# Optimization experiments

Measured on AMD Instinct MI355X. Metric: run time of the kernel, lower is better.

The kernel has to match this reference:

```python
import jax, jax.numpy as jnp
import numpy as np

B, LQ, LKV = 4, 512, 8192
Q_DIM, KV_DIM = 1024, 512
QK_CH, V_CH, N_HEADS = 256, 256, 8
EPS = 1e-5


def _layernorm(x, g, b):
    m = jnp.mean(x, axis=-1, keepdims=True)
    v = jnp.mean(jnp.square(x - m), axis=-1, keepdims=True)
    return (x - m) * jax.lax.rsqrt(v + EPS) * g + b


def setup_inputs() -> dict:
    key = jax.random.key(0)
    ks = jax.random.split(key, 8)
    hidden_states = jax.random.normal(ks[0], (B, LQ, Q_DIM), dtype=jnp.float32)
    inputs = jax.random.normal(ks[1], (B, LKV, KV_DIM), dtype=jnp.float32)
    # Linear weights stored as [in, out] for x @ W
    Wq = jax.random.normal(ks[2], (Q_DIM, QK_CH), dtype=jnp.float32) * (1.0 / np.sqrt(Q_DIM))
    Wk = jax.random.normal(ks[3], (KV_DIM, QK_CH), dtype=jnp.float32) * (1.0 / np.sqrt(KV_DIM))
    Wv = jax.random.normal(ks[4], (KV_DIM, V_CH), dtype=jnp.float32) * (1.0 / np.sqrt(KV_DIM))
    bq = jnp.zeros((QK_CH,), jnp.float32)
    bk = jax.random.normal(ks[5], (QK_CH,), dtype=jnp.float32) * 0.02
    bv = jax.random.normal(ks[6], (V_CH,), dtype=jnp.float32) * 0.02
    ln1_g = jnp.ones((Q_DIM,), jnp.float32)
    ln1_b = jnp.zeros((Q_DIM,), jnp.float32)
    ln2_g = jnp.ones((KV_DIM,), jnp.float32)
    ln2_b = jnp.zeros((KV_DIM,), jnp.float32)
    return dict(hidden_states=hidden_states, inputs=inputs,
                ln1_g=ln1_g, ln1_b=ln1_b, ln2_g=ln2_g, ln2_b=ln2_b,
                Wq=Wq, bq=bq, Wk=Wk, bk=bk, Wv=Wv, bv=bv)


def reference(hidden_states, inputs, ln1_g, ln1_b, ln2_g, ln2_b,
              Wq, bq, Wk, bk, Wv, bv):
    H = N_HEADS
    dqk = QK_CH // H
    dv = V_CH // H
    hs = _layernorm(hidden_states, ln1_g, ln1_b)          # [B,LQ,Q_DIM]
    inp = _layernorm(inputs, ln2_g, ln2_b)                # [B,LKV,KV_DIM]
    q = (hs @ Wq + bq).reshape(B, LQ, H, dqk)             # [B,LQ,H,dqk]
    k = (inp @ Wk + bk).reshape(B, LKV, H, dqk)           # [B,LKV,H,dqk]
    v = (inp @ Wv + bv).reshape(B, LKV, H, dv)            # [B,LKV,H,dv]
    scores = jnp.einsum('bqhd,bkhd->bhqk', q, k) / np.sqrt(dqk).astype(np.float32)
    probs = jax.nn.softmax(scores, axis=-1)               # [B,H,LQ,LKV] (materialized, as in torch)
    ctx = jnp.einsum('bhqk,bkhd->bqhd', probs, v)         # [B,LQ,H,dv]
    return ctx.reshape(B, LQ, H * dv)
```

## Files before the change

### kernel.cpp

```cpp
#include <hip/hip_runtime.h>
#include <hip/hip_bf16.h>
#include <math.h>

#define NB    4
#define LQ    512
#define LKV   8192
#define QDIM  1024
#define KVDIM 512
#define NH    8
#define EPS_LN 1e-5f
#define SMAX  12.0f

typedef __attribute__((ext_vector_type(8))) short bf16x8;
typedef __attribute__((ext_vector_type(4))) float f32x4;

static __device__ __forceinline__ ushort f2bf(float x) {
    unsigned int u = __builtin_bit_cast(unsigned int, x);
    u += 0x7FFFu + ((u >> 16) & 1u);
    return (ushort)(u >> 16);
}

#if __has_builtin(__builtin_amdgcn_cvt_pk_bf16_f32)
static __device__ __forceinline__ unsigned int pk_bf16(float a, float b) {
    auto r = __builtin_amdgcn_cvt_pk_bf16_f32(a, b);
    return __builtin_bit_cast(unsigned int, r);
}
#else
static __device__ __forceinline__ unsigned int pk_bf16(float a, float b) {
    return (unsigned int)f2bf(a) | ((unsigned int)f2bf(b) << 16);
}
#endif

#if __has_builtin(__builtin_amdgcn_exp2f)
#define EXP2F(x) __builtin_amdgcn_exp2f(x)
#else
#define EXP2F(x) exp2f(x)
#endif

static __device__ __forceinline__ void interleave_swap(unsigned int &x, unsigned int &y, int lane) {
#if __has_builtin(__builtin_amdgcn_permlane32_swap) && __has_builtin(__builtin_amdgcn_permlane16_swap)
    {
        auto r1 = __builtin_amdgcn_permlane32_swap(x, y, false, false);
        auto r2 = __builtin_amdgcn_permlane16_swap(r1[0], r1[1], false, false);
        x = (unsigned int)r2[0];
        y = (unsigned int)r2[1];
    }
#else
    {
        unsigned int xs = (unsigned int)__shfl_xor((int)x, 32, 64);
        unsigned int ys = (unsigned int)__shfl_xor((int)y, 32, 64);
        unsigned int A2 = (lane & 32) ? ys : x;
        unsigned int C2 = (lane & 32) ? y  : xs;
        unsigned int A2x = (unsigned int)__shfl_xor((int)A2, 16, 64);
        unsigned int C2x = (unsigned int)__shfl_xor((int)C2, 16, 64);
        x = (lane & 16) ? C2x : A2;
        y = (lane & 16) ? C2  : A2x;
    }
#endif
}

static __device__ __forceinline__ void gld_lds16(const ushort* g, ushort* l) {
    __builtin_amdgcn_global_load_lds(
        (const __attribute__((address_space(1))) unsigned int*)g,
        (__attribute__((address_space(3))) unsigned int*)l, 16, 0, 0);
}

template<int K>
static __device__ __forceinline__ void ln_norm_row(
    const float* __restrict__ x, const float* __restrict__ g,
    const float* __restrict__ bta, ushort* __restrict__ y, int row, int lane)
{
    const float* xp = x + (size_t)row * K;
    constexpr int NV = K / 256;
    float4 v[NV];
    float s = 0.f;
#pragma unroll
    for (int i = 0; i < NV; ++i) {
        v[i] = *(const float4*)(xp + lane * 4 + i * 256);
        s += v[i].x + v[i].y + v[i].z + v[i].w;
    }
#pragma unroll
    for (int o = 1; o < 64; o <<= 1) s += __shfl_xor(s, o, 64);
    const float mu = s * (1.0f / K);
    float vs = 0.f;
#pragma unroll
    for (int i = 0; i < NV; ++i) {
        float dx = v[i].x - mu, dy = v[i].y - mu, dz = v[i].z - mu, dw = v[i].w - mu;
        vs += dx * dx + dy * dy + dz * dz + dw * dw;
    }
#pragma unroll
    for (int o = 1; o < 64; o <<= 1) vs += __shfl_xor(vs, o, 64);
    const float rs = rsqrtf(vs * (1.0f / K) + EPS_LN);
#pragma unroll
    for (int i = 0; i < NV; ++i) {
        const float4 gv = *(const float4*)(g   + lane * 4 + i * 256);
        const float4 bv = *(const float4*)(bta + lane * 4 + i * 256);
        uint2 o;
        o.x = pk_bf16((v[i].x - mu) * rs * gv.x + bv.x, (v[i].y - mu) * rs * gv.y + bv.y);
        o.y = pk_bf16((v[i].z - mu) * rs * gv.z + bv.z, (v[i].w - mu) * rs * gv.w + bv.w);
        *(uint2*)(y + (size_t)row * K + lane * 4 + i * 256) = o;
    }
}

static __device__ __forceinline__ void ln_stats_row(
    const float* __restrict__ x, float* __restrict__ mean, float* __restrict__ rstd,
    int row, int lane)
{
    const float* xp = x + (size_t)row * QDIM;
    float4 v[4];
    float s = 0.f;
#pragma unroll
    for (int i = 0; i < 4; ++i) {
        v[i] = *(const float4*)(xp + lane * 4 + i * 256);
        s += v[i].x + v[i].y + v[i].z + v[i].w;
    }
#pragma unroll
    for (int o = 1; o < 64; o <<= 1) s += __shfl_xor(s, o, 64);
    const float mu = s * (1.0f / QDIM);
    float vs = 0.f;
#pragma unroll
    for (int i = 0; i < 4; ++i) {
        float dx = v[i].x - mu, dy = v[i].y - mu, dz = v[i].z - mu, dw = v[i].w - mu;
        vs += dx * dx + dy * dy + dz * dz + dw * dw;
    }
#pragma unroll
    for (int o = 1; o < 64; o <<= 1) vs += __shfl_xor(vs, o, 64);
    if (lane == 0) {
        mean[row] = mu;
        rstd[row] = rsqrtf(vs * (1.0f / QDIM) + EPS_LN);
    }
}

static __device__ __forceinline__ void wt_transpose_body(
    const float* __restrict__ src, ushort* __restrict__ dst, int K,
    int kx, int ny, int t, ushort (*Ts)[72])
{
    const int k0 = kx * 64, n0 = ny * 64;
    const int nl = t & 63;
#pragma unroll
    for (int p = 0; p < 16; ++p) {
        const int kl = p * 4 + (t >> 6);
        Ts[nl][kl] = f2bf(src[(size_t)(k0 + kl) * 256 + n0 + nl]);
    }
    __syncthreads();
    const int ck = (t & 7) * 8;
#pragma unroll
    for (int p = 0; p < 2; ++p) {
        const int rn = p * 32 + (t >> 3);
        *(bf16x8*)(dst + (size_t)(n0 + rn) * K + k0 + ck) = *(const bf16x8*)&Ts[rn][ck];
    }
}

__global__ __launch_bounds__(256) void phaseA_kernel(
    const float* __restrict__ inputs, const float* __restrict__ ln2g,
    const float* __restrict__ ln2b,   ushort* __restrict__ Abf,
    const float* __restrict__ hidden, float* __restrict__ mean_h, float* __restrict__ rstd_h,
    const float* __restrict__ Wq, const float* __restrict__ Wk, const float* __restrict__ Wv,
    ushort* __restrict__ WtQ, ushort* __restrict__ WtKV)
{
    __shared__ ushort Ts[64][72];
    const int bid = blockIdx.x;
    const int t = threadIdx.x;
    const int lane = t & 63;
    if (bid < 8192) {
        ln_norm_row<KVDIM>(inputs, ln2g, ln2b, Abf, bid * 4 + (t >> 6), lane);
    } else if (bid < 8704) {
        ln_stats_row(hidden, mean_h, rstd_h, (bid - 8192) * 4 + (t >> 6), lane);
    } else if (bid < 8768) {
        const int p = bid - 8704;
        wt_transpose_body(Wq, WtQ, QDIM, p & 15, p >> 4, t, Ts);
    } else if (bid < 8800) {
        const int p = bid - 8768;
        wt_transpose_body(Wk, WtKV, KVDIM, p & 7, p >> 3, t, Ts);
    } else {
        const int p = bid - 8800;
        wt_transpose_body(Wv, WtKV + (size_t)256 * KVDIM, KVDIM, p & 7, p >> 3, t, Ts);
    }
}

__global__ __launch_bounds__(256) void phaseB_kernel(
    const ushort* __restrict__ Abf, const ushort* __restrict__ WtKV,
    const float* __restrict__ bk, const float* __restrict__ bv,
    ushort* __restrict__ kb, ushort* __restrict__ vt,
    const float* __restrict__ hidden, const float* __restrict__ mean_h,
    const float* __restrict__ rstd_h,
    const float* __restrict__ ln1g, const float* __restrict__ ln1b,
    const ushort* __restrict__ WtQ, const float* __restrict__ bq,
    ushort* __restrict__ qb, float oscale)
{
    __shared__ __align__(16) ushort SMEM[4 * 64 * 72];
    const int bid  = blockIdx.x;
    const int t    = threadIdx.x;
    const int lane = t & 63;
    const int w    = t >> 6;
    const int lq   = lane & 15;
    const int lg   = lane >> 4;
    const int wm   = w >> 1;
    const int wn   = w & 1;

    if (bid < 1024) {
        const int bm = (bid >> 2) * 128;
        const int bn = (bid & 3) * 128;
        ushort* As = SMEM;
        ushort* Bs = SMEM + 8192;

        const int srow = t >> 3;
        const int scol = ((t & 7) ^ (srow & 7)) * 8;
        const ushort* gA = Abf  + (size_t)(bm + srow) * KVDIM + scol;
        const ushort* gB = WtKV + (size_t)(bn + srow) * KVDIM + scol;

        f32x4 acc[4][4] = {};
        for (int k0 = 0; k0 < KVDIM; k0 += 64) {
#pragma unroll
            for (int p = 0; p < 4; ++p) {
                gld_lds16(gA + (size_t)(p * 32) * KVDIM + k0, As + p * 2048 + t * 8);
                gld_lds16(gB + (size_t)(p * 32) * KVDIM + k0, Bs + p * 2048 + t * 8);
            }
            __syncthreads();
#pragma unroll
            for (int kh = 0; kh < 2; ++kh) {
                bf16x8 af[4], bf[4];
#pragma unroll
                for (int mt = 0; mt < 4; ++mt) {
                    const int m = wm * 64 + mt * 16 + lq;
                    af[mt] = *(const bf16x8*)(As + m * 64 + (((lg + 4 * kh) ^ (m & 7)) << 3));
                }
#pragma unroll
                for (int nt = 0; nt < 4; ++nt) {
                    const int n = wn * 64 + nt * 16 + lq;
                    bf[nt] = *(const bf16x8*)(Bs + n * 64 + (((lg + 4 * kh) ^ (n & 7)) << 3));
                }
#pragma unroll
                for (int mt = 0; mt < 4; ++mt)
#pragma unroll
                    for (int nt = 0; nt < 4; ++nt)
                        acc[mt][nt] = __builtin_amdgcn_mfma_f32_16x16x32_bf16(af[mt], bf[nt], acc[mt][nt], 0, 0, 0);
            }
            __syncthreads();
        }
        const int m0base = bm + wm * 64;
        const int bidx   = m0base >> 13;
        const int tokb   = m0base & 8191;

        if (bn < 256) {
            ushort (*Cs)[72] = (ushort(*)[72])(SMEM + w * 64 * 72);
#pragma unroll
            for (int nt = 0; nt < 4; ++nt) {
                const int n_l = nt * 16 + lq;
                const float bias = bk[bn + wn * 64 + n_l];
#pragma unroll
                for (int mt = 0; mt < 4; ++mt)
#pragma unroll
                    for (int r = 0; r < 4; ++r)
                        Cs[mt * 16 + lg * 4 + r][n_l] = f2bf(acc[mt][nt][r] + bias);
            }
            const int r0 = lane >> 3;
            const int ck = (lane & 7) * 8;
            const int nc = bn + wn * 64 + ck;
            const int h = nc >> 5, d = nc & 31;
            const size_t obase = (((size_t)(bidx * NH + h) << 13) + tokb) * 32 + d;
#pragma unroll
            for (int p = 0; p < 8; ++p) {
                const int row = p * 8 + r0;
                *(bf16x8*)(kb + obase + (size_t)row * 32) = *(const bf16x8*)&Cs[row][ck];
            }
        } else {
            ushort (*Cs)[72] = (ushort(*)[72])(SMEM + w * 64 * 72);
#pragma unroll
            for (int nt = 0; nt < 4; ++nt) {
                const int n_l = nt * 16 + lq;
                const float bias = bv[(bn - 256) + wn * 64 + n_l];
#pragma unroll
                for (int mt = 0; mt < 4; ++mt) {
                    uint2 o;
                    o.x = pk_bf16(acc[mt][nt][0] + bias, acc[mt][nt][1] + bias);
                    o.y = pk_bf16(acc[mt][nt][2] + bias, acc[mt][nt][3] + bias);
                    *(uint2*)&Cs[n_l][mt * 16 + lg * 4] = o;
                }
            }
            const int r0 = lane >> 3;
            const int cm = (lane & 7) * 8;
            const int tokc = tokb + cm;
#pragma unroll
            for (int p = 0; p < 8; ++p) {
                const int row = p * 8 + r0;
                const int nv  = (bn - 256) + wn * 64 + row;
                const int h = nv >> 5, d = nv & 31;
                *(bf16x8*)(vt + ((size_t)(bidx * NH + h) * 32 + d) * LKV + tokc) =
                    *(const bf16x8*)&Cs[row][cm];
            }
        }
    } else {
        const int p  = bid - 1024;
        const int bm = (p >> 2) * 64;
        const int bn = (p & 3) * 64;
        ushort* As = SMEM;
        ushort* Bs = SMEM + 4096;

        const int srow = t >> 3;
        const int scol = ((t & 7) ^ (srow & 7)) * 8;
        const ushort* gB = WtQ + (size_t)(bn + srow) * QDIM + scol;
        ushort* lB  = Bs + t * 8;
        ushort* lA0 = As + t * 8;
        ushort* lA1 = As + 2048 + t * 8;

        const int r0 = bm + srow;
        const float mu0 = mean_h[r0],      rs0 = rstd_h[r0];
        const float mu1 = mean_h[r0 + 32], rs1 = rstd_h[r0 + 32];
        const float* xA0 = hidden + (size_t)r0 * QDIM + scol;
        const float* xA1 = xA0 + (size_t)32 * QDIM;

        f32x4 acc[2][2] = {};
        for (int k0 = 0; k0 < QDIM; k0 += 64) {
            gld_lds16(gB + k0,                      lB);
            gld_lds16(gB + (size_t)32 * QDIM + k0,  lB + 2048);
            const float4 a0 = *(const float4*)(xA0 + k0);
            const float4 a1 = *(const float4*)(xA0 + k0 + 4);
            const float4 c0 = *(const float4*)(xA1 + k0);
            const float4 c1 = *(const float4*)(xA1 + k0 + 4);
            const float4 g0 = *(const float4*)(ln1g + k0 + scol);
            const float4 g1 = *(const float4*)(ln1g + k0 + scol + 4);
            const float4 d0 = *(const float4*)(ln1b + k0 + scol);
            const float4 d1 = *(const float4*)(ln1b + k0 + scol + 4);
            uint4 w0, w1;
            w0.x = pk_bf16((a0.x - mu0) * rs0 * g0.x + d0.x, (a0.y - mu0) * rs0 * g0.y + d0.y);
            w0.y = pk_bf16((a0.z - mu0) * rs0 * g0.z + d0.z, (a0.w - mu0) * rs0 * g0.w + d0.w);
            w0.z = pk_bf16((a1.x - mu0) * rs0 * g1.x + d1.x, (a1.y - mu0) * rs0 * g1.y + d1.y);
            w0.w = pk_bf16((a1.z - mu0) * rs0 * g1.z + d1.z, (a1.w - mu0) * rs0 * g1.w + d1.w);
            w1.x = pk_bf16((c0.x - mu1) * rs1 * g0.x + d0.x, (c0.y - mu1) * rs1 * g0.y + d0.y);
            w1.y = pk_bf16((c0.z - mu1) * rs1 * g0.z + d0.z, (c0.w - mu1) * rs1 * g0.w + d0.w);
            w1.z = pk_bf16((c1.x - mu1) * rs1 * g1.x + d1.x, (c1.y - mu1) * rs1 * g1.y + d1.y);
            w1.w = pk_bf16((c1.z - mu1) * rs1 * g1.z + d1.z, (c1.w - mu1) * rs1 * g1.w + d1.w);
            *(uint4*)lA0 = w0;
            *(uint4*)lA1 = w1;
            __syncthreads();
#pragma unroll
            for (int kh = 0; kh < 2; ++kh) {
                bf16x8 af[2], bf[2];
#pragma unroll
                for (int mt = 0; mt < 2; ++mt) {
                    const int m = wm * 32 + mt * 16 + lq;
                    af[mt] = *(const bf16x8*)(As + m * 64 + (((lg + 4 * kh) ^ (m & 7)) << 3));
                }
#pragma unroll
                for (int nt = 0; nt < 2; ++nt) {
                    const int n = wn * 32 + nt * 16 + lq;
                    bf[nt] = *(const bf16x8*)(Bs + n * 64 + (((lg + 4 * kh) ^ (n & 7)) << 3));
                }
#pragma unroll
                for (int mt = 0; mt < 2; ++mt)
#pragma unroll
                    for (int nt = 0; nt < 2; ++nt)
                        acc[mt][nt] = __builtin_amdgcn_mfma_f32_16x16x32_bf16(af[mt], bf[nt], acc[mt][nt], 0, 0, 0);
            }
            __syncthreads();
        }

#pragma unroll
        for (int nt = 0; nt < 2; ++nt) {
            const int n = bn + wn * 32 + nt * 16 + lq;
            const int h = n >> 5, d = n & 31;
            const float bias = bq[n];
#pragma unroll
            for (int mt = 0; mt < 2; ++mt) {
                const int m0   = bm + wm * 32 + mt * 16 + lg * 4;
                const int bidx = m0 >> 9;
                const int tok  = m0 & 511;
                const size_t base = (((size_t)(bidx * NH + h) << 9) + tok) * 32 + d;
#pragma unroll
                for (int r = 0; r < 4; ++r)
                    qb[base + (size_t)r * 32] = f2bf((acc[mt][nt][r] + bias) * oscale);
            }
        }
    }
}

__global__ __launch_bounds__(256, 4) void attn_mfma_kernel(
    const ushort* __restrict__ Qb,
    const ushort* __restrict__ Kb,
    const ushort* __restrict__ Vt,
    float* __restrict__ Opart,
    float* __restrict__ lpart)
{
    const int bid = blockIdx.x;
    const int xcd = bid & 7;
    const int u   = bid >> 3;
    const int bhw = u >> 6;
    const int r2  = u & 63;
    const int qt  = r2 >> 2;
    const int quarter = r2 & 3;
    const int bh  = (bhw << 3) | xcd;
    const int t = threadIdx.x, w = t >> 6, lane = t & 63;
    const int lq = lane & 15, lg = lane >> 4;

    __shared__ __align__(16) float Ob[2 * 32 * 36];
    __shared__ float lbuf[4][32];

    bf16x8 qfrag[2];
    const size_t qbase = ((size_t)bh * LQ + qt * 32) * 32;
    qfrag[0] = *(const bf16x8*)(Qb + qbase + (size_t)lq * 32 + lg * 8);
    qfrag[1] = *(const bf16x8*)(Qb + qbase + (size_t)(16 + lq) * 32 + lg * 8);

    const int kv0 = quarter * 2048 + w * 512;
    const ushort* KpA = Kb + ((size_t)bh * LKV + kv0 + lq) * 32 + lg * 8;
    const ushort* VpA = Vt + ((size_t)bh * 32 + lq) * LKV + kv0 + lg * 8;

    f32x4 oacc[2][2] = {};
    float l_part[2] = {0.f, 0.f};
    const f32x4 cM = {-SMAX, -SMAX, -SMAX, -SMAX};

    bf16x8 kf[4];
#pragma unroll
    for (int m = 0; m < 4; ++m)
        kf[m] = *(const bf16x8*)(KpA + (size_t)(m * 16) * 32);

    for (int kt = 0; kt < 512; kt += 64) {
        bf16x8 kc[4];
#pragma unroll
        for (int m = 0; m < 4; ++m) kc[m] = kf[m];

        bf16x8 vc[2][2];
#pragma unroll
        for (int dt = 0; dt < 2; ++dt)
#pragma unroll
            for (int hf = 0; hf < 2; ++hf)
                vc[dt][hf] = *(const bf16x8*)(VpA + (size_t)(dt * 16) * LKV + kt + hf * 32);

        const int nk = (kt + 64 < 512) ? kt + 64 : 0;
#pragma unroll
        for (int m = 0; m < 4; ++m)
            kf[m] = *(const bf16x8*)(KpA + (size_t)(nk + m * 16) * 32);

        f32x4 s[4][2];
#pragma unroll
        for (int m = 0; m < 4; ++m)
#pragma unroll
            for (int n = 0; n < 2; ++n)
                s[m][n] = __builtin_amdgcn_mfma_f32_16x16x32_bf16(kc[m], qfrag[n], cM, 0, 0, 0);

        bf16x8 pf[2][2];
#pragma unroll
        for (int n = 0; n < 2; ++n) {
#pragma unroll
            for (int z = 0; z < 2; ++z) {
                const float e0 = EXP2F(s[2 * z][n][0]);
                const float e1 = EXP2F(s[2 * z][n][1]);
                const float e2 = EXP2F(s[2 * z][n][2]);
                const float e3 = EXP2F(s[2 * z][n][3]);
                const float f0 = EXP2F(s[2 * z + 1][n][0]);
                const float f1 = EXP2F(s[2 * z + 1][n][1]);
                const float f2 = EXP2F(s[2 * z + 1][n][2]);
                const float f3 = EXP2F(s[2 * z + 1][n][3]);
                l_part[n] += ((e0 + e1) + (e2 + e3)) + ((f0 + f1) + (f2 + f3));
                unsigned int wa = pk_bf16(e0, e1);
                unsigned int wb = pk_bf16(e2, e3);
                unsigned int wc = pk_bf16(f0, f1);
                unsigned int wd = pk_bf16(f2, f3);
                interleave_swap(wa, wc, lane);
                interleave_swap(wb, wd, lane);
                uint4 wv;
                wv.x = wa; wv.y = wb; wv.z = wc; wv.w = wd;
                pf[n][z] = __builtin_bit_cast(bf16x8, wv);
            }
        }

#pragma unroll
        for (int dt = 0; dt < 2; ++dt)
#pragma unroll
            for (int n = 0; n < 2; ++n) {
                oacc[dt][n] = __builtin_amdgcn_mfma_f32_16x16x32_bf16(vc[dt][0], pf[n][0], oacc[dt][n], 0, 0, 0);
                oacc[dt][n] = __builtin_amdgcn_mfma_f32_16x16x32_bf16(vc[dt][1], pf[n][1], oacc[dt][n], 0, 0, 0);
            }
    }

#pragma unroll
    for (int n = 0; n < 2; ++n) {
        l_part[n] += __shfl_xor(l_part[n], 16);
        l_part[n] += __shfl_xor(l_part[n], 32);
    }
    if (lg == 0) {
        lbuf[w][lq]      = l_part[0];
        lbuf[w][16 + lq] = l_part[1];
    }
    if (w >= 2) {
#pragma unroll
        for (int n = 0; n < 2; ++n)
#pragma unroll
            for (int dt = 0; dt < 2; ++dt)
                *(f32x4*)&Ob[((size_t)(w - 2) * 32 + n * 16 + lq) * 36 + dt * 16 + lg * 4] = oacc[dt][n];
    }
    __syncthreads();
    if (w < 2) {
#pragma unroll
        for (int n = 0; n < 2; ++n)
#pragma unroll
            for (int dt = 0; dt < 2; ++dt) {
                float* p = &Ob[((size_t)w * 32 + n * 16 + lq) * 36 + dt * 16 + lg * 4];
                f32x4 v = *(f32x4*)p;
                v += oacc[dt][n];
                *(f32x4*)p = v;
            }
    }
    __syncthreads();
    {
        const int pidx = (quarter * 32 + bh) * 16 + qt;
        const int q  = t >> 3;
        const int d0 = (t & 7) * 4;
        f32x4 s0 = *(const f32x4*)&Ob[((size_t)q) * 36 + d0];
        f32x4 s1 = *(const f32x4*)&Ob[((size_t)(32 + q)) * 36 + d0];
        s0 += s1;
        *(f32x4*)(Opart + (size_t)pidx * 1024 + q * 32 + d0) = s0;
        if ((t & 7) == 0) {
            float gl = lbuf[0][q] + lbuf[1][q] + lbuf[2][q] + lbuf[3][q];
            lpart[(size_t)pidx * 32 + q] = gl;
        }
    }
}

__global__ __launch_bounds__(256) void attn_combine_kernel(
    const float* __restrict__ Opart, const float* __restrict__ lpart,
    float* __restrict__ Out)
{
    const int cb = blockIdx.x;
    const int bh = cb >> 4, qt = cb & 15;
    const int b = bh >> 3, h = bh & 7;
    const int t = threadIdx.x;
    const int q = t >> 3;
    const int dq = (t & 7) * 4;
    float4 o = {0.f, 0.f, 0.f, 0.f};
    float l = 0.f;
#pragma unroll
    for (int j = 0; j < 4; ++j) {
        const size_t pidx = (size_t)((j * 32 + bh) * 16 + qt);
        const float4 a = *(const float4*)(Opart + pidx * 1024 + q * 32 + dq);
        o.x += a.x; o.y += a.y; o.z += a.z; o.w += a.w;
        l += lpart[pidx * 32 + q];
    }
    const float inv = 1.0f / l;
    o.x *= inv; o.y *= inv; o.z *= inv; o.w *= inv;
    *(float4*)(Out + ((size_t)b * LQ + qt * 32 + q) * 256 + h * 32 + dq) = o;
}

extern "C" void kernel_launch(void* const* d_in, const int* in_sizes, int n_in,
                              void* d_out, int out_size, void* d_ws, size_t ws_size,
                              hipStream_t stream)
{
    const float* hidden = (const float*)d_in[0];
    const float* inputs = (const float*)d_in[1];
    const float* ln1g   = (const float*)d_in[2];
    const float* ln1b   = (const float*)d_in[3];
    const float* ln2g   = (const float*)d_in[4];
    const float* ln2b   = (const float*)d_in[5];
    const float* Wq     = (const float*)d_in[6];
    const float* bq     = (const float*)d_in[7];
    const float* Wk     = (const float*)d_in[8];
    const float* bk     = (const float*)d_in[9];
    const float* Wv     = (const float*)d_in[10];
    const float* bv     = (const float*)d_in[11];
    float* out = (float*)d_out;

    char* wsb = (char*)d_ws;
    ushort* qb     = (ushort*)(wsb);
    ushort* WtKV   = (ushort*)(wsb + (1u << 20));
    ushort* WtQ    = (ushort*)(wsb + (1u << 20) + (512u << 10));
    float*  mean_h = (float*)(wsb + (2u << 20));
    float*  rstd_h = (float*)(wsb + (2u << 20) + 8192);
    ushort* kb     = (ushort*)(wsb + (2u << 20) + 16384);
    ushort* vt     = (ushort*)(wsb + (18u << 20) + 16384);
    ushort* Abf    = (ushort*)(wsb + (34u << 20) + 16384);

    float* Opart = (float*)Abf;
    float* lpart = Opart + (size_t)4 * 32 * 16 * 1024;

    const float oscale = 0.2550540226496112f;

    phaseA_kernel<<<8832, 256, 0, stream>>>(inputs, ln2g, ln2b, Abf,
                                            hidden, mean_h, rstd_h,
                                            Wq, Wk, Wv, WtQ, WtKV);
    phaseB_kernel<<<1152, 256, 0, stream>>>(Abf, WtKV, bk, bv, kb, vt,
                                            hidden, mean_h, rstd_h, ln1g, ln1b,
                                            WtQ, bq, qb, oscale);
    attn_mfma_kernel<<<2048, 256, 0, stream>>>(qb, kb, vt, Opart, lpart);
    attn_combine_kernel<<<512, 256, 0, stream>>>(Opart, lpart, out);
}
```

Baseline: 215.8 us.

## Double query tile per attention block to reuse K/V loads across 64 queries

Measured after the change: 207.4 us. -3.9%, faster.

```diff
diff --git a/kernel.cpp b/kernel.cpp
--- a/kernel.cpp
+++ b/kernel.cpp
@@ -375,7 +375,8 @@
     }
 }
 
-__global__ __launch_bounds__(256, 4) void attn_mfma_kernel(
+#define NQ 4
+__global__ __launch_bounds__(256, 3) void attn_mfma_kernel(
     const ushort* __restrict__ Qb,
     const ushort* __restrict__ Kb,
     const ushort* __restrict__ Vt,
@@ -385,72 +386,63 @@
     const int bid = blockIdx.x;
     const int xcd = bid & 7;
     const int u   = bid >> 3;
-    const int bhw = u >> 6;
-    const int r2  = u & 63;
+    const int bhw = u >> 5;
+    const int r2  = u & 31;
     const int qt  = r2 >> 2;
     const int quarter = r2 & 3;
     const int bh  = (bhw << 3) | xcd;
     const int t = threadIdx.x, w = t >> 6, lane = t & 63;
     const int lq = lane & 15, lg = lane >> 4;
 
-    __shared__ __align__(16) float Ob[2 * 32 * 36];
-    __shared__ float lbuf[4][32];
-
-    bf16x8 qfrag[2];
-    const size_t qbase = ((size_t)bh * LQ + qt * 32) * 32;
-    qfrag[0] = *(const bf16x8*)(Qb + qbase + (size_t)lq * 32 + lg * 8);
-    qfrag[1] = *(const bf16x8*)(Qb + qbase + (size_t)(16 + lq) * 32 + lg * 8);
+    __shared__ __align__(16) float Ob[2 * 64 * 36];
+    __shared__ float lbuf[4][64];
+
+    bf16x8 qfrag[NQ];
+    const size_t qbase = ((size_t)bh * LQ + qt * 64) * 32;
+#pragma unroll
+    for (int n = 0; n < NQ; ++n)
+        qfrag[n] = *(const bf16x8*)(Qb + qbase + (size_t)(n * 16 + lq) * 32 + lg * 8);
 
     const int kv0 = quarter * 2048 + w * 512;
     const ushort* KpA = Kb + ((size_t)bh * LKV + kv0 + lq) * 32 + lg * 8;
     const ushort* VpA = Vt + ((size_t)bh * 32 + lq) * LKV + kv0 + lg * 8;
 
-    f32x4 oacc[2][2] = {};
-    float l_part[2] = {0.f, 0.f};
+    f32x4 oacc[2][NQ] = {};
+    float l_part[NQ] = {};
     const f32x4 cM = {-SMAX, -SMAX, -SMAX, -SMAX};
-
-    bf16x8 kf[4];
-#pragma unroll
-    for (int m = 0; m < 4; ++m)
-        kf[m] = *(const bf16x8*)(KpA + (size_t)(m * 16) * 32);
 
     for (int kt = 0; kt < 512; kt += 64) {
         bf16x8 kc[4];
 #pragma unroll
-        for (int m = 0; m < 4; ++m) kc[m] = kf[m];
-
+        for (int m = 0; m < 4; ++m)
+            kc[m] = *(const bf16x8*)(KpA + (size_t)(kt + m * 16) * 32);
         bf16x8 vc[2][2];
 #pragma unroll
         for (int dt = 0; dt < 2; ++dt)
 #pragma unroll
-            for (int hf = 0; hf < 2; ++hf)
-                vc[dt][hf] = *(const bf16x8*)(VpA + (size_t)(dt * 16) * LKV + kt + hf * 32);
-
-        const int nk = (kt + 64 < 512) ? kt + 64 : 0;
-#pragma unroll
-        for (int m = 0; m < 4; ++m)
-            kf[m] = *(const bf16x8*)(KpA + (size_t)(nk + m * 16) * 32);
-
-        f32x4 s[4][2];
-#pragma unroll
-        for (int m = 0; m < 4; ++m)
-#pragma unroll
-            for (int n = 0; n < 2; ++n)
-                s[m][n] = __builtin_amdgcn_mfma_f32_16x16x32_bf16(kc[m], qfrag[n], cM, 0, 0, 0);
-
-        bf16x8 pf[2][2];
-#pragma unroll
-        for (int n = 0; n < 2; ++n) {
-#pragma unroll
-            for (int z = 0; z < 2; ++z) {
-                const float e0 = EXP2F(s[2 * z][n][0]);
-                const float e1 = EXP2F(s[2 * z][n][1]);
-                const float e2 = EXP2F(s[2 * z][n][2]);
-                const float e3 = EXP2F(s[2 * z][n][3]);
-                const float f0 = EXP2F(s[2 * z + 1][n][0]);
-                const float f1 = EXP2F(s[2 * z + 1][n][1]);
-                const float f2 = EXP2F(s[2 * z + 1][n][2]);
-                const float f3 = EXP2F(s[2 * z + 1][n][3]);
+            for (int z = 0; z < 2; ++z)
+                vc[dt][z] = *(const bf16x8*)(VpA + (size_t)(dt * 16) * LKV + kt + z * 32);
+
+#pragma unroll
+        for (int z = 0; z < 2; ++z) {
+            f32x4 s2[2][NQ];
+#pragma unroll
+            for (int mm = 0; mm < 2; ++mm)
+#pragma unroll
+                for (int n = 0; n < NQ; ++n)
+                    s2[mm][n] = __builtin_amdgcn_mfma_f32_16x16x32_bf16(kc[2 * z + mm], qfrag[n], cM, 0, 0, 0);
+
+            bf16x8 pfz[NQ];
+#pragma unroll
+            for (int n = 0; n < NQ; ++n) {
+                const float e0 = EXP2F(s2[0][n][0]);
+                const float e1 = EXP2F(s2[0][n][1]);
+                const float e2 = EXP2F(s2[0][n][2]);
+                const float e3 = EXP2F(s2[0][n][3]);
+                const float f0 = EXP2F(s2[1][n][0]);
+                const float f1 = EXP2F(s2[1][n][1]);
+                const float f2 = EXP2F(s2[1][n][2]);
+                const float f3 = EXP2F(s2[1][n][3]);
                 l_part[n] += ((e0 + e1) + (e2 + e3)) + ((f0 + f1) + (f2 + f3));
                 unsigned int wa = pk_bf16(e0, e1);
                 unsigned int wb = pk_bf16(e2, e3);
@@ -460,42 +452,41 @@
                 interleave_swap(wb, wd, lane);
                 uint4 wv;
                 wv.x = wa; wv.y = wb; wv.z = wc; wv.w = wd;
-                pf[n][z] = __builtin_bit_cast(bf16x8, wv);
-            }
-        }
-
-#pragma unroll
-        for (int dt = 0; dt < 2; ++dt)
-#pragma unroll
-            for (int n = 0; n < 2; ++n) {
-                oacc[dt][n] = __builtin_amdgcn_mfma_f32_16x16x32_bf16(vc[dt][0], pf[n][0], oacc[dt][n], 0, 0, 0);
-                oacc[dt][n] = __builtin_amdgcn_mfma_f32_16x16x32_bf16(vc[dt][1], pf[n][1], oacc[dt][n], 0, 0, 0);
-            }
-    }
-
-#pragma unroll
-    for (int n = 0; n < 2; ++n) {
+                pfz[n] = __builtin_bit_cast(bf16x8, wv);
+            }
+
+#pragma unroll
+            for (int dt = 0; dt < 2; ++dt)
+#pragma unroll
+                for (int n = 0; n < NQ; ++n)
+                    oacc[dt][n] = __builtin_amdgcn_mfma_f32_16x16x32_bf16(vc[dt][z], pfz[n], oacc[dt][n], 0, 0, 0);
+        }
+    }
+
+#pragma unroll
+    for (int n = 0; n < NQ; ++n) {
         l_part[n] += __shfl_xor(l_part[n], 16);
         l_part[n] += __shfl_xor(l_part[n], 32);
     }
     if (lg == 0) {
-        lbuf[w][lq]      = l_part[0];
-        lbuf[w][16 + lq] = l_part[1];
+#pragma unroll
+        for (int n = 0; n < NQ; ++n)
+            lbuf[w][n * 16 + lq] = l_part[n];
     }
     if (w >= 2) {
 #pragma unroll
-        for (int n = 0; n < 2; ++n)
+        for (int n = 0; n < NQ; ++n)
 #pragma unroll
             for (int dt = 0; dt < 2; ++dt)
-                *(f32x4*)&Ob[((size_t)(w - 2) * 32 + n * 16 + lq) * 36 + dt * 16 + lg * 4] = oacc[dt][n];
+                *(f32x4*)&Ob[((size_t)(w - 2) * 64 + n * 16 + lq) * 36 + dt * 16 + lg * 4] = oacc[dt][n];
     }
     __syncthreads();
     if (w < 2) {
 #pragma unroll
-        for (int n = 0; n < 2; ++n)
+        for (int n = 0; n < NQ; ++n)
 #pragma unroll
             for (int dt = 0; dt < 2; ++dt) {
-                float* p = &Ob[((size_t)w * 32 + n * 16 + lq) * 36 + dt * 16 + lg * 4];
+                float* p = &Ob[((size_t)w * 64 + n * 16 + lq) * 36 + dt * 16 + lg * 4];
                 f32x4 v = *(f32x4*)p;
                 v += oacc[dt][n];
                 *(f32x4*)p = v;
@@ -503,16 +494,20 @@
     }
     __syncthreads();
     {
-        const int pidx = (quarter * 32 + bh) * 16 + qt;
+        const int pidx = (quarter * 32 + bh) * 8 + qt;
         const int q  = t >> 3;
         const int d0 = (t & 7) * 4;
-        f32x4 s0 = *(const f32x4*)&Ob[((size_t)q) * 36 + d0];
-        f32x4 s1 = *(const f32x4*)&Ob[((size_t)(32 + q)) * 36 + d0];
-        s0 += s1;
-        *(f32x4*)(Opart + (size_t)pidx * 1024 + q * 32 + d0) = s0;
-        if ((t & 7) == 0) {
-            float gl = lbuf[0][q] + lbuf[1][q] + lbuf[2][q] + lbuf[3][q];
-            lpart[(size_t)pidx * 32 + q] = gl;
+#pragma unroll
+        for (int rh = 0; rh < 2; ++rh) {
+            const int row = q + rh * 32;
+            f32x4 s0 = *(const f32x4*)&Ob[((size_t)row) * 36 + d0];
+            f32x4 s1 = *(const f32x4*)&Ob[((size_t)(64 + row)) * 36 + d0];
+            s0 += s1;
+            *(f32x4*)(Opart + (size_t)pidx * 2048 + row * 32 + d0) = s0;
+            if ((t & 7) == 0) {
+                float gl = lbuf[0][row] + lbuf[1][row] + lbuf[2][row] + lbuf[3][row];
+                lpart[(size_t)pidx * 64 + row] = gl;
+            }
         }
     }
 }
@@ -522,23 +517,27 @@
     float* __restrict__ Out)
 {
     const int cb = blockIdx.x;
-    const int bh = cb >> 4, qt = cb & 15;
+    const int bh = cb >> 3, qt = cb & 7;
     const int b = bh >> 3, h = bh & 7;
     const int t = threadIdx.x;
     const int q = t >> 3;
     const int dq = (t & 7) * 4;
-    float4 o = {0.f, 0.f, 0.f, 0.f};
-    float l = 0.f;
-#pragma unroll
-    for (int j = 0; j < 4; ++j) {
-        const size_t pidx = (size_t)((j * 32 + bh) * 16 + qt);
-        const float4 a = *(const float4*)(Opart + pidx * 1024 + q * 32 + dq);
-        o.x += a.x; o.y += a.y; o.z += a.z; o.w += a.w;
-        l += lpart[pidx * 32 + q];
-    }
-    const float inv = 1.0f / l;
-    o.x *= inv; o.y *= inv; o.z *= inv; o.w *= inv;
-    *(float4*)(Out + ((size_t)b * LQ + qt * 32 + q) * 256 + h * 32 + dq) = o;
+#pragma unroll
+    for (int rh = 0; rh < 2; ++rh) {
+        const int row = q + rh * 32;
+        float4 o = {0.f, 0.f, 0.f, 0.f};
+        float l = 0.f;
+#pragma unroll
+        for (int j = 0; j < 4; ++j) {
+            const size_t pidx = (size_t)((j * 32 + bh) * 8 + qt);
+            const float4 a = *(const float4*)(Opart + pidx * 2048 + row * 32 + dq);
+            o.x += a.x; o.y += a.y; o.z += a.z; o.w += a.w;
+            l += lpart[pidx * 64 + row];
+        }
+        const float inv = 1.0f / l;
+        o.x *= inv; o.y *= inv; o.z *= inv; o.w *= inv;
+        *(float4*)(Out + ((size_t)b * LQ + qt * 64 + row) * 256 + h * 32 + dq) = o;
+    }
 }
 
 extern "C" void kernel_launch(void* const* d_in, const int* in_sizes, int n_in,
@@ -570,7 +569,7 @@
     ushort* Abf    = (ushort*)(wsb + (34u << 20) + 16384);
 
     float* Opart = (float*)Abf;
-    float* lpart = Opart + (size_t)4 * 32 * 16 * 1024;
+    float* lpart = Opart + (size_t)4 * 32 * 8 * 2048;
 
     const float oscale = 0.2550540226496112f;
 
@@ -580,6 +579,6 @@
     phaseB_kernel<<<1152, 256, 0, stream>>>(Abf, WtKV, bk, bv, kb, vt,
                                             hidden, mean_h, rstd_h, ln1g, ln1b,
                                             WtQ, bq, qb, oscale);
-    attn_mfma_kernel<<<2048, 256, 0, stream>>>(qb, kb, vt, Opart, lpart);
-    attn_combine_kernel<<<512, 256, 0, stream>>>(Opart, lpart, out);
-}
+    attn_mfma_kernel<<<1024, 256, 0, stream>>>(qb, kb, vt, Opart, lpart);
+    attn_combine_kernel<<<256, 256, 0, stream>>>(Opart, lpart, out);
+}
```
